# Kernel optimization log

Hardware: AMD Instinct MI355X
Metric: run time of the kernel (lower is better)

Reference implementation:

```python
import jax, jax.numpy as jnp
import numpy as np

N_NODES = 100000
N_EDGES = 1600000
N_GRAPHS = 64
F_IN = 256
HID = 256
PROJ = 128
L = 4


def setup_inputs() -> dict:
    key = jax.random.key(0)
    ks = jax.random.split(key, 12)
    x = jax.random.normal(ks[0], (N_NODES, F_IN), dtype=jnp.float32)
    edge_index = jax.random.randint(ks[1], (2, N_EDGES), 0, N_NODES)
    batch = jnp.sort(jax.random.randint(ks[2], (N_NODES,), 0, N_GRAPHS))
    s = 0.05
    # SAGEConv per layer: lin_l (applied to mean-aggregated neighbors, with bias)
    # and lin_r (applied to root node, no bias). All layers are 256->256, stacked.
    Wl = jax.random.normal(ks[3], (L, HID, HID), dtype=jnp.float32) * s
    bl = jax.random.normal(ks[4], (L, HID), dtype=jnp.float32) * s
    Wr = jax.random.normal(ks[5], (L, HID, HID), dtype=jnp.float32) * s
    gamma = jnp.ones((L, HID), dtype=jnp.float32)
    beta = jnp.zeros((L, HID), dtype=jnp.float32)
    W1 = jax.random.normal(ks[6], (HID, HID), dtype=jnp.float32) * s
    b1 = jnp.zeros((HID,), dtype=jnp.float32)
    W2 = jax.random.normal(ks[7], (HID, PROJ), dtype=jnp.float32) * s
    b2 = jnp.zeros((PROJ,), dtype=jnp.float32)
    return {"x": x, "edge_index": edge_index, "batch": batch,
            "Wl": Wl, "bl": bl, "Wr": Wr, "gamma": gamma, "beta": beta,
            "W1": W1, "b1": b1, "W2": W2, "b2": b2}


def _segment_mean(vals, seg_ids, num_segments):
    sums = jax.ops.segment_sum(vals, seg_ids, num_segments=num_segments)
    cnt = jax.ops.segment_sum(jnp.ones((vals.shape[0],), vals.dtype), seg_ids,
                              num_segments=num_segments)
    return sums / jnp.maximum(cnt, 1.0)[:, None]


def reference(x, edge_index, batch, Wl, bl, Wr, gamma, beta, W1, b1, W2, b2):
    src, dst = edge_index[0], edge_index[1]
    eps = 1e-5
    h = x
    for i in range(L):
        # SAGEConv: mean-aggregate neighbor features, then lin_l(aggr) + lin_r(root)
        aggr = _segment_mean(h[src], dst, N_NODES)          # [N, HID]
        h = aggr @ Wl[i] + bl[i] + h @ Wr[i]
        # BatchNorm1d (training-mode batch statistics, biased variance)
        mu = jnp.mean(h, axis=0)
        var = jnp.mean(jnp.square(h - mu), axis=0)
        h = (h - mu) * jax.lax.rsqrt(var + eps) * gamma[i] + beta[i]
        h = jax.nn.relu(h)
        # dropout omitted (inference / deterministic reference)
    g = _segment_mean(h, batch, N_GRAPHS)                   # [G, HID]
    z = jax.nn.relu(g @ W1 + b1) @ W2 + b2                  # [G, PROJ]
    # F.normalize(z, dim=1): L2 normalize with eps clamp
    norm = jnp.maximum(jnp.linalg.norm(z, axis=1, keepdims=True), 1e-12)
    return z / norm
```

## Files before the change

### kernel.cpp

```cpp
#include <hip/hip_runtime.h>

#define N_NODES 100000
#define M_PAD   100096
#define N_MBLK  782
#define N_EDGES 1600000
#define N_GRAPHS 64
#define HID 256
#define PROJ 128
#define NLAYERS 4

#define EBUF_STRIDE 8192
#define N_BUCKETS ((N_NODES + 255) / 256)
#define CSR_BLK 1024
#define EPT 10
#define CSR_NBLK ((N_EDGES + CSR_BLK * EPT - 1) / (CSR_BLK * EPT))
#define SENT 0xFFFFFFFFu

typedef unsigned short u16;
typedef unsigned long long u64;
typedef __attribute__((ext_vector_type(4))) float f32x4;
typedef __attribute__((ext_vector_type(2))) float vf2;

__device__ __forceinline__ float b2f_lo(unsigned u) {
  return __uint_as_float(u << 16);
}
__device__ __forceinline__ float b2f_hi(unsigned u) {
  return __uint_as_float(u & 0xFFFF0000u);
}
__device__ __forceinline__ u16 f2b(float f) {
  unsigned u = __float_as_uint(f);
  u = (u + 0x7FFF + ((u >> 16) & 1)) >> 16;
  return (u16)u;
}
__device__ __forceinline__ void gload16(const void* g, void* l) {
  __builtin_amdgcn_global_load_lds((const __attribute__((address_space(1))) void*)g,
                                   (__attribute__((address_space(3))) void*)l, 16, 0, 0);
}
__device__ __forceinline__ unsigned pack_fp8x4(float a, float b, float c, float d) {
  int v = __builtin_amdgcn_cvt_pk_fp8_f32(a, b, 0, false);
  v = __builtin_amdgcn_cvt_pk_fp8_f32(c, d, v, true);
  return (unsigned)v;
}
__device__ __forceinline__ void accf8(float* a, unsigned w) {
  vf2 lo = __builtin_amdgcn_cvt_pk_f32_fp8((int)w, false);
  vf2 hi = __builtin_amdgcn_cvt_pk_f32_fp8((int)w, true);
  a[0] += lo.x; a[1] += lo.y; a[2] += hi.x; a[3] += hi.y;
}

__global__ __launch_bounds__(1024) void bucket_scatter(
    const int* __restrict__ src, const int* __restrict__ dst,
    u64* __restrict__ bfill64, uint2* __restrict__ ebuf) {
  __shared__ int lhist[N_BUCKETS];
  __shared__ int lbase[N_BUCKETS];
  int t = threadIdx.x;
  int e0 = blockIdx.x * (CSR_BLK * EPT) + t;
  for (int i = t; i < N_BUCKETS; i += CSR_BLK) lhist[i] = 0;
  __syncthreads();
  int sv[EPT], dv[EPT];
#pragma unroll
  for (int j = 0; j < EPT; j++) {
    int e = e0 + j * CSR_BLK;
    if (e < N_EDGES) {
      sv[j] = src[e];
      dv[j] = dst[e];
      atomicAdd(&lhist[dv[j] >> 8], 1);
    } else {
      dv[j] = -1;
      sv[j] = 0;
    }
  }
  __syncthreads();
  for (int i = t; i < N_BUCKETS; i += CSR_BLK) {
    int c = lhist[i];
    if (c > 0) {
      int rounded = (c + 7) & ~7;
      u64 old = atomicAdd(&bfill64[(size_t)i * 8],
                          ((u64)rounded << 32) | (u64)c);
      int base = (int)(old >> 32);
      lbase[i] = base;
      for (int k = c; k < rounded; k++) {
        int p = base + k;
        if (p < EBUF_STRIDE) {
          uint2 q; q.x = 0; q.y = SENT;
          ebuf[(size_t)i * EBUF_STRIDE + p] = q;
        }
      }
      lhist[i] = 0;
    }
  }
  __syncthreads();
#pragma unroll
  for (int j = 0; j < EPT; j++) {
    if (dv[j] >= 0) {
      int b = dv[j] >> 8;
      int p = lbase[b] + atomicAdd(&lhist[b], 1);
      if (p < EBUF_STRIDE) {
        uint2 q;
        q.x = (unsigned)sv[j];
        q.y = (unsigned)dv[j];
        ebuf[(size_t)b * EBUF_STRIDE + p] = q;
      }
    }
  }
}

__global__ __launch_bounds__(512) void bucket_prefix(
    const u64* __restrict__ bfill64, int* __restrict__ bucket_base,
    int* __restrict__ row_ptr) {
  __shared__ int tile[512];
  int t = threadIdx.x;
  int v = 0;
  if (t < N_BUCKETS) {
    u64 w = bfill64[(size_t)t * 8];
    v = (int)(w & 0xFFFFFFFFull);
    if ((int)(w >> 32) > EBUF_STRIDE) v = min(v, EBUF_STRIDE);
  }
  tile[t] = v;
  __syncthreads();
  for (int off = 1; off < 512; off <<= 1) {
    int add = (t >= off) ? tile[t - off] : 0;
    __syncthreads();
    tile[t] += add;
    __syncthreads();
  }
  if (t < N_BUCKETS) bucket_base[t] = tile[t] - v;
  if (t == N_BUCKETS - 1) row_ptr[N_NODES] = tile[t];
}

__global__ __launch_bounds__(1024) void csr_build(
    const uint2* __restrict__ ebuf, const u64* __restrict__ bfill64,
    const int* __restrict__ bucket_base, int* __restrict__ row_ptr,
    float* __restrict__ inv_cnt, int* __restrict__ col) {
  __shared__ int hist[256];
  __shared__ int nscan[256];
  __shared__ int cursor[256];
  int b = blockIdx.x;
  int t = threadIdx.x;
  int nalloc = min((int)(bfill64[(size_t)b * 8] >> 32), EBUF_STRIDE);
  int bbase = bucket_base[b];
  if (t < 256) hist[t] = 0;
  __syncthreads();
  uint2 q[8];
#pragma unroll
  for (int k = 0; k < 8; k++) {
    int i = t + k * CSR_BLK;
    q[k].x = 0; q[k].y = SENT;
    if (i < nalloc) {
      q[k] = ebuf[(size_t)b * EBUF_STRIDE + i];
      if (q[k].y != SENT) atomicAdd(&hist[q[k].y & 255], 1);
    }
  }
  __syncthreads();
  if (t < 256) nscan[t] = hist[t];
  __syncthreads();
  for (int off = 1; off < 256; off <<= 1) {
    int add = 0;
    if (t < 256 && t >= off) add = nscan[t - off];
    __syncthreads();
    if (t < 256) nscan[t] += add;
    __syncthreads();
  }
  int nb = min(256, N_NODES - b * 256);
  if (t < 256) {
    int excl = nscan[t] - hist[t];
    cursor[t] = excl;
    if (t < nb) {
      row_ptr[b * 256 + t] = bbase + excl;
      inv_cnt[b * 256 + t] = 1.0f / fmaxf((float)hist[t], 1.0f);
    }
  }
  __syncthreads();
#pragma unroll
  for (int k = 0; k < 8; k++) {
    if (q[k].y != SENT) {
      int l = (int)(q[k].y & 255);
      int pos = bbase + atomicAdd(&cursor[l], 1);
      col[pos] = (int)q[k].x;
    }
  }
}

__global__ __launch_bounds__(256) void convert_x8(const float4* __restrict__ x,
                                                  unsigned* __restrict__ h8) {
  int i = blockIdx.x * blockDim.x + threadIdx.x;
  float4 v = x[i];
  h8[i] = pack_fp8x4(v.x, v.y, v.z, v.w);
}

__global__ __launch_bounds__(256) void convert_w8(const float* __restrict__ Wl,
                                                  const float* __restrict__ Wr,
                                                  unsigned* __restrict__ Wt8) {
  int idx = blockIdx.x * blockDim.x + threadIdx.x;
  int l = idx >> 15;
  int r = idx & 32767;
  int n = r >> 7;
  int k4 = (r & 127) * 4;
  float v[4];
#pragma unroll
  for (int j = 0; j < 4; j++) {
    int k = k4 + j;
    v[j] = (k < 256) ? Wl[(size_t)l * 65536 + k * 256 + n]
                     : Wr[(size_t)l * 65536 + (k - 256) * 256 + n];
  }
  Wt8[idx] = pack_fp8x4(v[0], v[1], v[2], v[3]);
}

__global__ __launch_bounds__(256) void aggregate_fp8(
    const unsigned char* __restrict__ h8, const int* __restrict__ row_ptr,
    const int* __restrict__ col, const float* __restrict__ inv_cnt,
    unsigned char* __restrict__ aggr8) {
  int node = blockIdx.x * 4 + (threadIdx.x >> 6);
  int lane = threadIdx.x & 63;
  int half = lane >> 5, l32 = lane & 31;
  int r0 = row_ptr[node], r1 = row_ptr[node + 1];
  float a[8] = {0.f, 0.f, 0.f, 0.f, 0.f, 0.f, 0.f, 0.f};
  int e = r0 + half;
  for (; e + 14 < r1; e += 16) {
    int s[8];
#pragma unroll
    for (int j = 0; j < 8; j++) s[j] = col[e + 2 * j];
    uint2 v[8];
#pragma unroll
    for (int j = 0; j < 8; j++)
      v[j] = *((const uint2*)(h8 + (size_t)s[j] * HID) + l32);
#pragma unroll
    for (int j = 0; j < 8; j++) { accf8(a, v[j].x); accf8(a + 4, v[j].y); }
  }
  for (; e + 6 < r1; e += 8) {
    int s0 = col[e], s1 = col[e + 2], s2 = col[e + 4], s3 = col[e + 6];
    uint2 v0 = *((const uint2*)(h8 + (size_t)s0 * HID) + l32);
    uint2 v1 = *((const uint2*)(h8 + (size_t)s1 * HID) + l32);
    uint2 v2 = *((const uint2*)(h8 + (size_t)s2 * HID) + l32);
    uint2 v3 = *((const uint2*)(h8 + (size_t)s3 * HID) + l32);
    accf8(a, v0.x); accf8(a + 4, v0.y);
    accf8(a, v1.x); accf8(a + 4, v1.y);
    accf8(a, v2.x); accf8(a + 4, v2.y);
    accf8(a, v3.x); accf8(a + 4, v3.y);
  }
  for (; e < r1; e += 2) {
    int s0 = col[e];
    uint2 v0 = *((const uint2*)(h8 + (size_t)s0 * HID) + l32);
    accf8(a, v0.x); accf8(a + 4, v0.y);
  }
#pragma unroll
  for (int j = 0; j < 8; j++) a[j] += __shfl_xor(a[j], 32, 64);
  if (half == 0) {
    float inv = inv_cnt[node];
    uint2 o;
    o.x = pack_fp8x4(a[0] * inv, a[1] * inv, a[2] * inv, a[3] * inv);
    o.y = pack_fp8x4(a[4] * inv, a[5] * inv, a[6] * inv, a[7] * inv);
    *((uint2*)(aggr8 + (size_t)node * HID) + l32) = o;
  }
}

__global__ __launch_bounds__(256, 2) void gemm_fused_fp8(
    const unsigned char* __restrict__ a8, const unsigned char* __restrict__ h8,
    const unsigned char* __restrict__ Bt8, u16* __restrict__ hpre,
    float* __restrict__ psum) {
  __shared__ unsigned char smem[128 * 64 + 256 * 64];
  __shared__ float bns[4][8][16][2];
  unsigned char* As = smem;
  unsigned char* Bs = smem + 128 * 64;
  u16* ep = (u16*)smem;

  int tid = threadIdx.x;
  int wid = tid >> 6, lane = tid & 63;
  int m0 = blockIdx.x * 128;
  int q = lane >> 4, c = lane & 15;
  int wm = (wid >> 1) * 64, wn = (wid & 1) * 128;

  f32x4 zero = {0.f, 0.f, 0.f, 0.f};
  f32x4 acc[4][8];
#pragma unroll
  for (int mi = 0; mi < 4; mi++)
#pragma unroll
    for (int ni = 0; ni < 8; ni++) acc[mi][ni] = zero;

  int srowA0 = wid * 32 + (lane >> 2);
  int cgA0 = (lane & 3) ^ ((srowA0 >> 1) & 3);
  int srowA1 = srowA0 + 16;
  int cgA1 = (lane & 3) ^ ((srowA1 >> 1) & 3);
  int srowB[4], cgB[4];
#pragma unroll
  for (int j = 0; j < 4; j++) {
    srowB[j] = j * 64 + wid * 16 + (lane >> 2);
    cgB[j] = (lane & 3) ^ ((srowB[j] >> 1) & 3);
  }

  int aoff[4][2], boff[8][2];
#pragma unroll
  for (int mi = 0; mi < 4; mi++) {
    int row = wm + mi * 16 + c;
    int x = (row >> 1) & 3;
#pragma unroll
    for (int kk = 0; kk < 2; kk++) {
      int chunk = kk * 2 + (q >> 1);
      aoff[mi][kk] = row * 64 + ((chunk ^ x) << 4) + ((q & 1) << 3);
    }
  }
#pragma unroll
  for (int ni = 0; ni < 8; ni++) {
    int row = wn + ni * 16 + c;
    int x = (row >> 1) & 3;
#pragma unroll
    for (int kk = 0; kk < 2; kk++) {
      int chunk = kk * 2 + (q >> 1);
      boff[ni][kk] = row * 64 + ((chunk ^ x) << 4) + ((q & 1) << 3);
    }
  }

  for (int k0 = 0; k0 < 512; k0 += 64) {
    const unsigned char* Asrc = (k0 < 256) ? a8 : h8;
    int ksrc = k0 & 255;
    gload16(Asrc + ((size_t)(m0 + srowA0) * HID + ksrc + cgA0 * 16), &As[(wid * 32) * 64]);
    gload16(Asrc + ((size_t)(m0 + srowA1) * HID + ksrc + cgA1 * 16), &As[(wid * 32 + 16) * 64]);
#pragma unroll
    for (int j = 0; j < 4; j++)
      gload16(Bt8 + ((size_t)srowB[j] * 512 + k0 + cgB[j] * 16), &Bs[(j * 64 + wid * 16) * 64]);
    __syncthreads();
    long long af[4][2], bfr[8][2];
#pragma unroll
    for (int mi = 0; mi < 4; mi++) {
      af[mi][0] = *(const long long*)&As[aoff[mi][0]];
      af[mi][1] = *(const long long*)&As[aoff[mi][1]];
    }
#pragma unroll
    for (int ni = 0; ni < 8; ni++) {
      bfr[ni][0] = *(const long long*)&Bs[boff[ni][0]];
      bfr[ni][1] = *(const long long*)&Bs[boff[ni][1]];
    }
#pragma unroll
    for (int mi = 0; mi < 4; mi++)
#pragma unroll
      for (int ni = 0; ni < 8; ni++) {
        acc[mi][ni] = __builtin_amdgcn_mfma_f32_16x16x32_fp8_fp8(
            af[mi][0], bfr[ni][0], acc[mi][ni], 0, 0, 0);
        acc[mi][ni] = __builtin_amdgcn_mfma_f32_16x16x32_fp8_fp8(
            af[mi][1], bfr[ni][1], acc[mi][ni], 0, 0, 0);
      }
    __syncthreads();
  }

  int rh = wid >> 1;
#pragma unroll
  for (int mi = 0; mi < 4; mi++) {
#pragma unroll
    for (int r = 0; r < 4; r++) {
      int r16 = q * 4 + r;
#pragma unroll
      for (int ni = 0; ni < 8; ni++)
        ep[(rh * 16 + r16) * 256 + wn + ni * 16 + c] = f2b(acc[mi][ni][r]);
    }
    __syncthreads();
    int u = tid;
#pragma unroll
    for (int j = 0; j < 4; j++, u += 256) {
      int lr = u >> 5;
      int cu = u & 31;
      int gm = m0 + (lr >> 4) * 64 + mi * 16 + (lr & 15);
      if (gm < N_NODES)
        ((uint4*)(hpre + (size_t)gm * HID))[cu] = ((const uint4*)ep)[u];
    }
    __syncthreads();
  }

#pragma unroll
  for (int ni = 0; ni < 8; ni++) {
    float s = 0.f, s2 = 0.f;
#pragma unroll
    for (int mi = 0; mi < 4; mi++) {
#pragma unroll
      for (int r = 0; r < 4; r++) {
        int gm = m0 + wm + mi * 16 + q * 4 + r;
        float v = (gm < N_NODES) ? acc[mi][ni][r] : 0.f;
        s += v;
        s2 += v * v;
      }
    }
    s += __shfl_xor(s, 16, 64);
    s += __shfl_xor(s, 32, 64);
    s2 += __shfl_xor(s2, 16, 64);
    s2 += __shfl_xor(s2, 32, 64);
    if (q == 0) {
      bns[wid][ni][c][0] = s;
      bns[wid][ni][c][1] = s2;
    }
  }
  __syncthreads();
  {
    int wnh = tid >> 7, ni = (tid >> 4) & 7, cc = tid & 15;
    float s = bns[wnh][ni][cc][0] + bns[wnh + 2][ni][cc][0];
    float s2 = bns[wnh][ni][cc][1] + bns[wnh + 2][ni][cc][1];
    int coln = wnh * 128 + ni * 16 + cc;
    psum[(size_t)blockIdx.x * 512 + coln] = s;
    psum[(size_t)blockIdx.x * 512 + 256 + coln] = s2;
  }
}

#define BN_MID 16
__global__ __launch_bounds__(256) void bn_mid(const float* __restrict__ psum,
                                              float* __restrict__ tmp) {
  int b = blockIdx.x;
  int f = threadIdx.x;
  int mb0 = b * 49;
  int mb1 = min(mb0 + 49, N_MBLK);
  float s = 0.f, s2 = 0.f;
  for (int mb = mb0; mb < mb1; mb++) {
    s += psum[(size_t)mb * 512 + f];
    s2 += psum[(size_t)mb * 512 + 256 + f];
  }
  tmp[(size_t)b * 512 + f] = s;
  tmp[(size_t)b * 512 + 256 + f] = s2;
}

__global__ void bn_fin(const float* __restrict__ tmp,
                       const float* __restrict__ gamma,
                       const float* __restrict__ beta,
                       float* __restrict__ ss) {
  int f = threadIdx.x;
  float sum = 0.f, sq = 0.f;
#pragma unroll
  for (int b = 0; b < BN_MID; b++) {
    sum += tmp[(size_t)b * 512 + f];
    sq += tmp[(size_t)b * 512 + 256 + f];
  }
  const float invN = 1.0f / (float)N_NODES;
  float mu = sum * invN;
  float ex2 = sq * invN;
  float var = fmaxf(ex2 - mu * mu, 0.f);
  float sc = gamma[f] * rsqrtf(var + 1e-5f);
  ss[f] = sc;
  ss[HID + f] = beta[f] - mu * sc;
}

__global__ __launch_bounds__(256) void bn_apply_h8(const uint4* __restrict__ hpre,
                                                   const float* __restrict__ ss,
                                                   uint2* __restrict__ h8out) {
  int idx0 = blockIdx.x * blockDim.x + threadIdx.x;
  int cb = (idx0 & 31) * 8;
  float sc[8], sh[8];
#pragma unroll
  for (int j = 0; j < 8; j++) { sc[j] = ss[cb + j]; sh[j] = ss[HID + cb + j]; }
  const int total = N_NODES * 32;
  const int step = gridDim.x * blockDim.x;
  for (int i = idx0; i < total; i += step) {
    uint4 v = hpre[i];
    unsigned vv[4] = {v.x, v.y, v.z, v.w};
    float f[8];
#pragma unroll
    for (int j = 0; j < 4; j++) {
      f[2 * j]     = fmaxf(fmaf(b2f_lo(vv[j]), sc[2 * j], sh[2 * j]), 0.f);
      f[2 * j + 1] = fmaxf(fmaf(b2f_hi(vv[j]), sc[2 * j + 1], sh[2 * j + 1]), 0.f);
    }
    uint2 q;
    q.x = pack_fp8x4(f[0], f[1], f[2], f[3]);
    q.y = pack_fp8x4(f[4], f[5], f[6], f[7]);
    h8out[i] = q;
  }
}

__global__ __launch_bounds__(256) void pool_partial(
    const u16* __restrict__ hpre, const float* __restrict__ ss,
    const int* __restrict__ batch, float* __restrict__ partial) {
  __shared__ float red[256][9];
  int g = blockIdx.x;
  int i = blockIdx.y;
  int t = threadIdx.x;
  int a = 0, b = N_NODES;
  while (a < b) { int m = (a + b) >> 1; if (batch[m] < g) a = m + 1; else b = m; }
  int lo = a;
  b = N_NODES;
  while (a < b) { int m = (a + b) >> 1; if (batch[m] < g + 1) a = m + 1; else b = m; }
  int hi = a;
  int len = hi - lo;
  int clen = (len + 7) >> 3;
  int c0 = lo + i * clen;
  int c1 = min(c0 + clen, hi);

  int rs = t >> 5, cu = t & 31;
  int cb = cu * 8;
  float scv[8], shv[8];
#pragma unroll
  for (int j = 0; j < 8; j++) { scv[j] = ss[cb + j]; shv[j] = ss[HID + cb + j]; }
  float acc[8] = {0.f, 0.f, 0.f, 0.f, 0.f, 0.f, 0.f, 0.f};
  for (int r = c0 + rs; r < c1; r += 8) {
    uint4 v = *((const uint4*)(hpre + (size_t)r * HID) + cu);
    unsigned vv[4] = {v.x, v.y, v.z, v.w};
#pragma unroll
    for (int j = 0; j < 4; j++) {
      acc[2 * j]     += fmaxf(fmaf(b2f_lo(vv[j]), scv[2 * j], shv[2 * j]), 0.f);
      acc[2 * j + 1] += fmaxf(fmaf(b2f_hi(vv[j]), scv[2 * j + 1], shv[2 * j + 1]), 0.f);
    }
  }
#pragma unroll
  for (int j = 0; j < 8; j++) red[t][j] = acc[j];
  __syncthreads();
  int cc = t >> 3, j = t & 7;
  float sum = 0.f;
#pragma unroll
  for (int k = 0; k < 8; k++) sum += red[k * 32 + cc][j];
  partial[((size_t)g * 8 + i) * 256 + t] = sum;
}

__global__ __launch_bounds__(256) void pool_mlp_final(
    const float* __restrict__ partial, const int* __restrict__ batch,
    const float* __restrict__ W1, const float* __restrict__ b1,
    const float* __restrict__ W2, const float* __restrict__ b2,
    float* __restrict__ out) {
  __shared__ float gs[HID];
  __shared__ float ts[HID];
  __shared__ float rn[PROJ];
  int g = blockIdx.x;
  int t = threadIdx.x;
  int a = 0, b = N_NODES;
  while (a < b) { int m = (a + b) >> 1; if (batch[m] < g) a = m + 1; else b = m; }
  int lo = a;
  b = N_NODES;
  while (a < b) { int m = (a + b) >> 1; if (batch[m] < g + 1) a = m + 1; else b = m; }
  int len = a - lo;

  float sum = 0.f;
#pragma unroll
  for (int i = 0; i < 8; i++) sum += partial[((size_t)g * 8 + i) * 256 + t];
  float inv = 1.0f / fmaxf((float)len, 1.0f);
  gs[t] = sum * inv;
  __syncthreads();

  float s = b1[t];
  for (int k = 0; k < HID; k++) s = fmaf(gs[k], W1[(size_t)k * HID + t], s);
  ts[t] = fmaxf(s, 0.f);
  __syncthreads();
  float z = 0.f;
  if (t < PROJ) {
    z = b2[t];
    for (int k = 0; k < HID; k++) z = fmaf(ts[k], W2[(size_t)k * PROJ + t], z);
    rn[t] = z * z;
  }
  __syncthreads();
  for (int off = PROJ / 2; off > 0; off >>= 1) {
    if (t < off) rn[t] += rn[t + off];
    __syncthreads();
  }
  float norm = fmaxf(sqrtf(rn[0]), 1e-12f);
  if (t < PROJ) out[(size_t)g * PROJ + t] = z / norm;
}

extern "C" void kernel_launch(void* const* d_in, const int* in_sizes, int n_in,
                              void* d_out, int out_size, void* d_ws, size_t ws_size,
                              hipStream_t stream) {
  const float* x = (const float*)d_in[0];
  const int* ei = (const int*)d_in[1];
  const int* src = ei;
  const int* dst = ei + N_EDGES;
  const int* batch = (const int*)d_in[2];
  const float* Wl = (const float*)d_in[3];
  const float* Wr = (const float*)d_in[5];
  const float* gamma = (const float*)d_in[6];
  const float* beta = (const float*)d_in[7];
  const float* W1 = (const float*)d_in[8];
  const float* b1 = (const float*)d_in[9];
  const float* W2 = (const float*)d_in[10];
  const float* b2 = (const float*)d_in[11];
  float* out = (float*)d_out;

  char* p = (char*)d_ws;
  const size_t HB = (size_t)M_PAD * HID * sizeof(u16);
  const size_t H8 = (size_t)M_PAD * HID;
  u16* hpre = (u16*)p;   p += HB;
  unsigned char* aggr8 = (unsigned char*)p; p += H8;
  unsigned char* h8 = (unsigned char*)p;    p += H8;
  unsigned char* Wt8 = (unsigned char*)p;   p += (size_t)NLAYERS * 512 * HID;
  int* col = (int*)p;    p += (size_t)N_EDGES * sizeof(int);
  int* row_ptr = (int*)p; p += 400016;
  float* inv_cnt = (float*)p; p += (size_t)N_NODES * sizeof(float);
  float* psum = (float*)p;    p += (size_t)N_MBLK * 512 * sizeof(float);
  float* tmp = (float*)p;     p += (size_t)BN_MID * 512 * sizeof(float);
  float* ss = (float*)p;      p += 512 * sizeof(float);
  float* partial = (float*)p; p += (size_t)N_GRAPHS * 8 * 256 * sizeof(float);
  uint2* ebuf = (uint2*)p;    p += (size_t)N_BUCKETS * EBUF_STRIDE * sizeof(uint2);

  u64* bfill64 = (u64*)hpre;
  int* bucket_base = (int*)(bfill64 + (size_t)N_BUCKETS * 8);

  hipMemsetAsync(bfill64, 0, (size_t)N_BUCKETS * 8 * sizeof(u64), stream);
  bucket_scatter<<<CSR_NBLK, CSR_BLK, 0, stream>>>(src, dst, bfill64, ebuf);
  bucket_prefix<<<1, 512, 0, stream>>>(bfill64, bucket_base, row_ptr);
  csr_build<<<N_BUCKETS, CSR_BLK, 0, stream>>>(ebuf, bfill64, bucket_base,
                                               row_ptr, inv_cnt, col);

  convert_x8<<<N_NODES / 4, 256, 0, stream>>>((const float4*)x, (unsigned*)h8);
  convert_w8<<<(NLAYERS * 512 * HID / 4) / 256, 256, 0, stream>>>(Wl, Wr,
                                                                  (unsigned*)Wt8);

  for (int l = 0; l < NLAYERS; l++) {
    aggregate_fp8<<<N_NODES / 4, 256, 0, stream>>>(h8, row_ptr, col, inv_cnt, aggr8);
    gemm_fused_fp8<<<N_MBLK, 256, 0, stream>>>(aggr8, h8,
                                               Wt8 + (size_t)l * 512 * HID,
                                               hpre, psum);
    bn_mid<<<BN_MID, 256, 0, stream>>>(psum, tmp);
    bn_fin<<<1, 256, 0, stream>>>(tmp, gamma + (size_t)l * HID,
                                  beta + (size_t)l * HID, ss);
    if (l < NLAYERS - 1) {
      bn_apply_h8<<<2048, 256, 0, stream>>>((const uint4*)hpre, ss, (uint2*)h8);
    }
  }

  pool_partial<<<dim3(N_GRAPHS, 8), 256, 0, stream>>>(hpre, ss, batch, partial);
  pool_mlp_final<<<N_GRAPHS, 256, 0, stream>>>(partial, batch, W1, b1, W2, b2, out);
}
```

Before: 783.6 us.

## Store pre-BN activations in fp8 and double-buffer GEMM LDS stages

The GEMM epilogue now writes the pre-BatchNorm activations as fp8 instead of bf16, halving that buffer's write traffic and the reads in bn_apply and pool_partial. Both consumers decode fp8 instead of bf16. The GEMM K loop also gains a double-buffered LDS stage, so the next tile's global loads are issued before the current tile's MFMAs, hiding load latency. The cost is extra quantization error on pre-BN values, which carry unnormalized magnitudes in fp8, and roughly 48KB of LDS per block, which may strain the two-blocks-per-CU launch bound.

```diff
diff --git a/kernel.cpp b/kernel.cpp
--- a/kernel.cpp
+++ b/kernel.cpp
@@ -15,18 +15,13 @@
 #define EPT 10
 #define CSR_NBLK ((N_EDGES + CSR_BLK * EPT - 1) / (CSR_BLK * EPT))
 #define SENT 0xFFFFFFFFu
+#define GEMM_BUF 24576
 
 typedef unsigned short u16;
 typedef unsigned long long u64;
 typedef __attribute__((ext_vector_type(4))) float f32x4;
 typedef __attribute__((ext_vector_type(2))) float vf2;
 
-__device__ __forceinline__ float b2f_lo(unsigned u) {
-  return __uint_as_float(u << 16);
-}
-__device__ __forceinline__ float b2f_hi(unsigned u) {
-  return __uint_as_float(u & 0xFFFF0000u);
-}
 __device__ __forceinline__ u16 f2b(float f) {
   unsigned u = __float_as_uint(f);
   u = (u + 0x7FFF + ((u >> 16) & 1)) >> 16;
@@ -41,10 +36,18 @@
   v = __builtin_amdgcn_cvt_pk_fp8_f32(c, d, v, true);
   return (unsigned)v;
 }
+__device__ __forceinline__ unsigned char f2f8(float a) {
+  return (unsigned char)(__builtin_amdgcn_cvt_pk_fp8_f32(a, a, 0, false) & 0xFF);
+}
 __device__ __forceinline__ void accf8(float* a, unsigned w) {
   vf2 lo = __builtin_amdgcn_cvt_pk_f32_fp8((int)w, false);
   vf2 hi = __builtin_amdgcn_cvt_pk_f32_fp8((int)w, true);
   a[0] += lo.x; a[1] += lo.y; a[2] += hi.x; a[3] += hi.y;
+}
+__device__ __forceinline__ void decf8(float* f, unsigned w) {
+  vf2 lo = __builtin_amdgcn_cvt_pk_f32_fp8((int)w, false);
+  vf2 hi = __builtin_amdgcn_cvt_pk_f32_fp8((int)w, true);
+  f[0] = lo.x; f[1] = lo.y; f[2] = hi.x; f[3] = hi.y;
 }
 
 __global__ __launch_bounds__(1024) void bucket_scatter(
@@ -255,13 +258,10 @@
 
 __global__ __launch_bounds__(256, 2) void gemm_fused_fp8(
     const unsigned char* __restrict__ a8, const unsigned char* __restrict__ h8,
-    const unsigned char* __restrict__ Bt8, u16* __restrict__ hpre,
+    const unsigned char* __restrict__ Bt8, unsigned char* __restrict__ hpre8,
     float* __restrict__ psum) {
-  __shared__ unsigned char smem[128 * 64 + 256 * 64];
+  __shared__ unsigned char smem[2 * GEMM_BUF];
   __shared__ float bns[4][8][16][2];
-  unsigned char* As = smem;
-  unsigned char* Bs = smem + 128 * 64;
-  u16* ep = (u16*)smem;
 
   int tid = threadIdx.x;
   int wid = tid >> 6, lane = tid & 63;
@@ -309,15 +309,29 @@
     }
   }
 
-  for (int k0 = 0; k0 < 512; k0 += 64) {
+  auto stage = [&](int k0, int b) {
     const unsigned char* Asrc = (k0 < 256) ? a8 : h8;
     int ksrc = k0 & 255;
-    gload16(Asrc + ((size_t)(m0 + srowA0) * HID + ksrc + cgA0 * 16), &As[(wid * 32) * 64]);
-    gload16(Asrc + ((size_t)(m0 + srowA1) * HID + ksrc + cgA1 * 16), &As[(wid * 32 + 16) * 64]);
+    unsigned char* As = smem + b * GEMM_BUF;
+    unsigned char* Bs = As + 128 * 64;
+    gload16(Asrc + ((size_t)(m0 + srowA0) * HID + ksrc + cgA0 * 16),
+            &As[(wid * 32) * 64]);
+    gload16(Asrc + ((size_t)(m0 + srowA1) * HID + ksrc + cgA1 * 16),
+            &As[(wid * 32 + 16) * 64]);
 #pragma unroll
     for (int j = 0; j < 4; j++)
-      gload16(Bt8 + ((size_t)srowB[j] * 512 + k0 + cgB[j] * 16), &Bs[(j * 64 + wid * 16) * 64]);
-    __syncthreads();
+      gload16(Bt8 + ((size_t)srowB[j] * 512 + k0 + cgB[j] * 16),
+              &Bs[(j * 64 + wid * 16) * 64]);
+  };
+
+  stage(0, 0);
+  __syncthreads();
+#pragma unroll
+  for (int t = 0; t < 8; ++t) {
+    int cur = t & 1;
+    if (t < 7) stage((t + 1) * 64, cur ^ 1);
+    const unsigned char* As = smem + cur * GEMM_BUF;
+    const unsigned char* Bs = As + 128 * 64;
     long long af[4][2], bfr[8][2];
 #pragma unroll
     for (int mi = 0; mi < 4; mi++) {
@@ -341,6 +355,7 @@
     __syncthreads();
   }
 
+  unsigned char* ep8 = smem;
   int rh = wid >> 1;
 #pragma unroll
   for (int mi = 0; mi < 4; mi++) {
@@ -349,17 +364,17 @@
       int r16 = q * 4 + r;
 #pragma unroll
       for (int ni = 0; ni < 8; ni++)
-        ep[(rh * 16 + r16) * 256 + wn + ni * 16 + c] = f2b(acc[mi][ni][r]);
+        ep8[(rh * 16 + r16) * 256 + wn + ni * 16 + c] = f2f8(acc[mi][ni][r]);
     }
     __syncthreads();
     int u = tid;
 #pragma unroll
-    for (int j = 0; j < 4; j++, u += 256) {
-      int lr = u >> 5;
-      int cu = u & 31;
+    for (int j = 0; j < 2; j++, u += 256) {
+      int lr = u >> 4;
+      int cu = u & 15;
       int gm = m0 + (lr >> 4) * 64 + mi * 16 + (lr & 15);
       if (gm < N_NODES)
-        ((uint4*)(hpre + (size_t)gm * HID))[cu] = ((const uint4*)ep)[u];
+        ((uint4*)(hpre8 + (size_t)gm * HID))[cu] = ((const uint4*)ep8)[u];
     }
     __syncthreads();
   }
@@ -433,7 +448,7 @@
   ss[HID + f] = beta[f] - mu * sc;
 }
 
-__global__ __launch_bounds__(256) void bn_apply_h8(const uint4* __restrict__ hpre,
+__global__ __launch_bounds__(256) void bn_apply_h8(const uint2* __restrict__ hpre8,
                                                    const float* __restrict__ ss,
                                                    uint2* __restrict__ h8out) {
   int idx0 = blockIdx.x * blockDim.x + threadIdx.x;
@@ -444,23 +459,22 @@
   const int total = N_NODES * 32;
   const int step = gridDim.x * blockDim.x;
   for (int i = idx0; i < total; i += step) {
-    uint4 v = hpre[i];
-    unsigned vv[4] = {v.x, v.y, v.z, v.w};
+    uint2 v = hpre8[i];
     float f[8];
-#pragma unroll
-    for (int j = 0; j < 4; j++) {
-      f[2 * j]     = fmaxf(fmaf(b2f_lo(vv[j]), sc[2 * j], sh[2 * j]), 0.f);
-      f[2 * j + 1] = fmaxf(fmaf(b2f_hi(vv[j]), sc[2 * j + 1], sh[2 * j + 1]), 0.f);
-    }
-    uint2 q;
-    q.x = pack_fp8x4(f[0], f[1], f[2], f[3]);
-    q.y = pack_fp8x4(f[4], f[5], f[6], f[7]);
-    h8out[i] = q;
+    decf8(f, v.x);
+    decf8(f + 4, v.y);
+#pragma unroll
+    for (int j = 0; j < 8; j++)
+      f[j] = fmaxf(fmaf(f[j], sc[j], sh[j]), 0.f);
+    uint2 o;
+    o.x = pack_fp8x4(f[0], f[1], f[2], f[3]);
+    o.y = pack_fp8x4(f[4], f[5], f[6], f[7]);
+    h8out[i] = o;
   }
 }
 
 __global__ __launch_bounds__(256) void pool_partial(
-    const u16* __restrict__ hpre, const float* __restrict__ ss,
+    const unsigned char* __restrict__ hpre8, const float* __restrict__ ss,
     const int* __restrict__ batch, float* __restrict__ partial) {
   __shared__ float red[256][9];
   int g = blockIdx.x;
@@ -484,13 +498,13 @@
   for (int j = 0; j < 8; j++) { scv[j] = ss[cb + j]; shv[j] = ss[HID + cb + j]; }
   float acc[8] = {0.f, 0.f, 0.f, 0.f, 0.f, 0.f, 0.f, 0.f};
   for (int r = c0 + rs; r < c1; r += 8) {
-    uint4 v = *((const uint4*)(hpre + (size_t)r * HID) + cu);
-    unsigned vv[4] = {v.x, v.y, v.z, v.w};
-#pragma unroll
-    for (int j = 0; j < 4; j++) {
-      acc[2 * j]     += fmaxf(fmaf(b2f_lo(vv[j]), scv[2 * j], shv[2 * j]), 0.f);
-      acc[2 * j + 1] += fmaxf(fmaf(b2f_hi(vv[j]), scv[2 * j + 1], shv[2 * j + 1]), 0.f);
-    }
+    uint2 v = *((const uint2*)(hpre8 + (size_t)r * HID) + cu);
+    float f[8];
+    decf8(f, v.x);
+    decf8(f + 4, v.y);
+#pragma unroll
+    for (int j = 0; j < 8; j++)
+      acc[j] += fmaxf(fmaf(f[j], scv[j], shv[j]), 0.f);
   }
 #pragma unroll
   for (int j = 0; j < 8; j++) red[t][j] = acc[j];
@@ -564,9 +578,8 @@
   float* out = (float*)d_out;
 
   char* p = (char*)d_ws;
-  const size_t HB = (size_t)M_PAD * HID * sizeof(u16);
   const size_t H8 = (size_t)M_PAD * HID;
-  u16* hpre = (u16*)p;   p += HB;
+  unsigned char* hpre8 = (unsigned char*)p; p += H8;
   unsigned char* aggr8 = (unsigned char*)p; p += H8;
   unsigned char* h8 = (unsigned char*)p;    p += H8;
   unsigned char* Wt8 = (unsigned char*)p;   p += (size_t)NLAYERS * 512 * HID;
@@ -579,7 +592,7 @@
   float* partial = (float*)p; p += (size_t)N_GRAPHS * 8 * 256 * sizeof(float);
   uint2* ebuf = (uint2*)p;    p += (size_t)N_BUCKETS * EBUF_STRIDE * sizeof(uint2);
 
-  u64* bfill64 = (u64*)hpre;
+  u64* bfill64 = (u64*)hpre8;
   int* bucket_base = (int*)(bfill64 + (size_t)N_BUCKETS * 8);
 
   hipMemsetAsync(bfill64, 0, (size_t)N_BUCKETS * 8 * sizeof(u64), stream);
@@ -596,15 +609,15 @@
     aggregate_fp8<<<N_NODES / 4, 256, 0, stream>>>(h8, row_ptr, col, inv_cnt, aggr8);
     gemm_fused_fp8<<<N_MBLK, 256, 0, stream>>>(aggr8, h8,
                                                Wt8 + (size_t)l * 512 * HID,
-                                               hpre, psum);
+                                               hpre8, psum);
     bn_mid<<<BN_MID, 256, 0, stream>>>(psum, tmp);
     bn_fin<<<1, 256, 0, stream>>>(tmp, gamma + (size_t)l * HID,
                                   beta + (size_t)l * HID, ss);
     if (l < NLAYERS - 1) {
-      bn_apply_h8<<<2048, 256, 0, stream>>>((const uint4*)hpre, ss, (uint2*)h8);
-    }
-  }
-
-  pool_partial<<<dim3(N_GRAPHS, 8), 256, 0, stream>>>(hpre, ss, batch, partial);
+      bn_apply_h8<<<2048, 256, 0, stream>>>((const uint2*)hpre8, ss, (uint2*)h8);
+    }
+  }
+
+  pool_partial<<<dim3(N_GRAPHS, 8), 256, 0, stream>>>(hpre8, ss, batch, partial);
   pool_mlp_final<<<N_GRAPHS, 256, 0, stream>>>(partial, batch, W1, b1, W2, b2, out);
 }
```

Measured after the change: 770.8 us. No clear change (-1.6%).
